# Kernel tuning notes

Measured on AMD Instinct MI355X. Metric: run time of the kernel, lower is better.

## Reference

```python
import jax, jax.numpy as jnp
import numpy as np


def _segsum(v, idx, n):
    return jax.ops.segment_sum(v, idx, num_segments=n)


def _rdl(z, n_dst, Wna, We, Wi, es, ed, is_, id_):
    """Relationship_Decoupled_layer: node softmax attn + per-edge attn.
    e-channel (mode etype): softmax over 2 logits; i-channel: sigmoid(1 logit)."""
    zd = z[:n_dst]
    node_alpha = jax.nn.softmax(zd @ Wna, axis=1)                      # [nd,2]
    e_e = jax.nn.softmax(jnp.concatenate([z[es], zd[ed]], axis=-1) @ We, axis=1)  # [Ee,2]
    e_i = jax.nn.sigmoid(jnp.concatenate([z[is_], zd[id_]], axis=-1) @ Wi)        # [Ei,1]
    return node_alpha, e_e, e_i


def _one_agg(z, n_dst, W, b, na, e_e, es, ed):
    """One_Neighbor_Aggregation: mean over nbrs of e[:,0]*Linear(z_src), relu, + alpha0*z_dst.
    Linear is applied on src nodes once (linearity) instead of per-edge."""
    zd = na[:, 0:1] * z[:n_dst]
    wz = z @ W + b                                                     # [n_src,D]
    s = _segsum(e_e[:, 0:1] * wz[es], ed, n_dst)                       # [nd,D]
    deg = _segsum(jnp.ones((es.shape[0], 1), z.dtype), ed, n_dst)
    f = jax.nn.relu(s / jnp.maximum(deg, 1.0))
    return f + zd


def _nia(z, n_dst, na, e_e, es, ed, e_i, is_, id_):
    """Neighbor_Interaction_Aggregation: e_h (mode etype, attn col 1) and i_h
    (other etype, sigmoid attn), cross term via polarization identity, + alpha1*z_dst."""
    zd = na[:, 1:2] * z[:n_dst]
    e_h = _segsum(e_e[:, 1:2] * z[es], ed, n_dst)
    i_h = _segsum(e_i * z[is_], id_, n_dst)
    inter = jax.nn.relu(0.5 * (jnp.square(e_h + i_h) - jnp.square(e_h) - jnp.square(i_h)))
    return inter + zd


def setup_inputs() -> dict:
    key = jax.random.key(0)
    ks = jax.random.split(key, 32)
    F, D, O = 256, 128, 64
    n_src0, n_dst0, E0 = 100000, 25000, 500000
    n_src1, n_dst1, E1 = 25000, 5000, 100000

    def ri(k, n, hi):
        return jax.random.randint(k, (n,), 0, hi, dtype=jnp.int32)

    inp = {
        'feat': jax.random.normal(ks[0], (n_src0, F), jnp.float32),
        'src0_cor': ri(ks[1], E0, n_src0), 'dst0_cor': ri(ks[2], E0, n_dst0),
        'src0_sim': ri(ks[3], E0, n_src0), 'dst0_sim': ri(ks[4], E0, n_dst0),
        'src1_cor': ri(ks[5], E1, n_src1), 'dst1_cor': ri(ks[6], E1, n_dst1),
        'src1_sim': ri(ks[7], E1, n_src1), 'dst1_sim': ri(ks[8], E1, n_dst1),
        'n_dst0': n_dst0, 'n_dst1': n_dst1,
    }
    s = 0.05  # keep attention logits / activations in a sane range
    inp['Win'] = jax.random.normal(ks[9], (2, F, D)) * s
    inp['b_in'] = jnp.zeros((2, D), jnp.float32)
    inp['na1'] = jax.random.normal(ks[10], (2, D, 2)) * s
    inp['ea1'] = jax.random.normal(ks[11], (2, 2 * D, 2)) * s
    inp['ia1'] = jax.random.normal(ks[12], (2, 2 * D, 1)) * s
    inp['W1'] = jax.random.normal(ks[13], (2, D, D)) * s
    inp['b1'] = jnp.zeros((2, D), jnp.float32)
    inp['na2'] = jax.random.normal(ks[14], (2, D, 2)) * s
    inp['ea2'] = jax.random.normal(ks[15], (2, 2 * D, 2)) * s
    inp['ia2'] = jax.random.normal(ks[16], (2, 2 * D, 1)) * s
    inp['W2'] = jax.random.normal(ks[17], (2, D, D)) * s
    inp['b2'] = jnp.zeros((2, D), jnp.float32)
    inp['Wout'] = jax.random.normal(ks[18], (2, D, O)) * s
    inp['bout'] = jnp.zeros((2, O), jnp.float32)
    return inp


def reference(feat, src0_cor, dst0_cor, src0_sim, dst0_sim,
              src1_cor, dst1_cor, src1_sim, dst1_sim, n_dst0, n_dst1,
              Win, b_in, na1, ea1, ia1, W1, b1, na2, ea2, ia2, W2, b2, Wout, bout):
    # mode index 0 = 'cor', 1 = 'sim'; e-channel = mode etype, i-channel = other etype
    blk0 = {0: (src0_cor, dst0_cor, src0_sim, dst0_sim),
            1: (src0_sim, dst0_sim, src0_cor, dst0_cor)}
    blk1 = {0: (src1_cor, dst1_cor, src1_sim, dst1_sim),
            1: (src1_sim, dst1_sim, src1_cor, dst1_cor)}
    outs = []
    for m in range(2):
        es0, ed0, is0, id0 = blk0[m]
        es1, ed1, is1, id1 = blk1[m]
        z = feat @ Win[m] + b_in[m]                                    # fc_input (eval: dropout = identity)
        # layer 1 on block0
        na, ee, ei = _rdl(z, n_dst0, na1[m], ea1[m], ia1[m], es0, ed0, is0, id0)
        one = _one_agg(z, n_dst0, W1[m], b1[m], na, ee, es0, ed0)
        nia = _nia(z, n_dst0, na, ee, es0, ed0, ei, is0, id0)
        z = 0.5 * (one + nia)                                          # [n_dst0, D]
        # layer 2 on block1
        na, ee, ei = _rdl(z, n_dst1, na2[m], ea2[m], ia2[m], es1, ed1, is1, id1)
        one = _one_agg(z, n_dst1, W2[m], b2[m], na, ee, es1, ed1)
        nia = _nia(z, n_dst1, na, ee, es1, ed1, ei, is1, id1)
        z = 0.5 * (one + nia)                                          # [n_dst1, D]
        outs.append(z @ Wout[m] + bout[m])
    return jnp.stack(outs)                                             # [2, n_dst1, O] (cor, sim)
```

## Files before the change

### kernel.cpp

```cpp
#include <hip/hip_runtime.h>
#include <hip/hip_bf16.h>
#include <math.h>

#define F_DIM 256
#define D_DIM 128
#define O_DIM 64
#define NS0   100000
#define ND0   25000
#define E0_N  500000
#define NS1   25000
#define ND1   5000
#define E1_N  100000

#define NBE0  1954
#define NBE1  391
#define NB_CSR (2 * NBE0 + 2 * NBE1)
#define NB_WPREP 576

typedef __attribute__((ext_vector_type(8))) short s8v;
typedef __attribute__((ext_vector_type(4))) float f4v;

struct CPtr4 { const int *p0, *p1, *p2, *p3; };
struct MPtr4 { int *p0, *p1, *p2, *p3; };

__device__ __forceinline__ float2 unpack2(uint u) {
    union { uint i; float f; } a, b;
    a.i = (u & 0xffffu) << 16; b.i = u & 0xffff0000u;
    return make_float2(a.f, b.f);
}
__device__ __forceinline__ ushort f2bf(float f) {
    __hip_bfloat16 h = __float2bfloat16(f);
    return *(ushort*)&h;
}
__device__ __forceinline__ float u2f(uint u) {
    union { uint i; float f; } v; v.i = u; return v.f;
}
__device__ __forceinline__ uint f2u(float f) {
    union { uint i; float f; } v; v.f = f; return v.i;
}

__global__ __launch_bounds__(256) void gemm_l0(
    const float* __restrict__ A,
    const ushort* __restrict__ Btb,
    const float* __restrict__ biasb,
    ushort* __restrict__ Coutb, size_t coutstr, int M)
{
    constexpr int PA = 40;
    __shared__ ushort As[64 * PA];
    __shared__ ushort Bs[2][128 * PA];

    const int tid = threadIdx.x;
    const int row0 = blockIdx.x * 64;
    const int wave = tid >> 6, lane = tid & 63;
    const int l15 = lane & 15, l4 = lane >> 4;
    const int wm0 = (wave >> 1) * 32;
    const int wn0 = (wave & 1) * 64;

    f4v acc[2][2][4];
    #pragma unroll
    for (int m2 = 0; m2 < 2; ++m2)
        #pragma unroll
        for (int i = 0; i < 2; ++i)
            #pragma unroll
            for (int j = 0; j < 4; ++j)
                acc[m2][i][j] = (f4v)(0.0f);

    for (int kc = 0; kc < F_DIM; kc += 32) {
        __syncthreads();
        {
            int r = tid >> 2, g = (tid & 3) * 8;
            int gr = row0 + r;
            float4 v0 = make_float4(0.f, 0.f, 0.f, 0.f);
            float4 v1 = make_float4(0.f, 0.f, 0.f, 0.f);
            if (gr < M) {
                v0 = *(const float4*)(A + (size_t)gr * F_DIM + kc + g);
                v1 = *(const float4*)(A + (size_t)gr * F_DIM + kc + g + 4);
            }
            ushort4 o0, o1;
            o0.x = f2bf(v0.x); o0.y = f2bf(v0.y); o0.z = f2bf(v0.z); o0.w = f2bf(v0.w);
            o1.x = f2bf(v1.x); o1.y = f2bf(v1.y); o1.z = f2bf(v1.z); o1.w = f2bf(v1.w);
            *(ushort4*)(&As[r * PA + g]) = o0;
            *(ushort4*)(&As[r * PA + g + 4]) = o1;
        }
        #pragma unroll
        for (int m2 = 0; m2 < 2; ++m2)
            #pragma unroll
            for (int it = 0; it < 2; ++it) {
                int f = tid + it * 256;
                int r = f >> 2, g = (f & 3) * 8;
                *(float4*)(&Bs[m2][r * PA + g]) =
                    *(const float4*)(Btb + m2 * (D_DIM * F_DIM) + (size_t)r * F_DIM + kc + g);
            }
        __syncthreads();

        s8v af[2];
        #pragma unroll
        for (int i = 0; i < 2; ++i)
            af[i] = *(const s8v*)(&As[(wm0 + i * 16 + l15) * PA + l4 * 8]);
        #pragma unroll
        for (int m2 = 0; m2 < 2; ++m2) {
            s8v bfr[4];
            #pragma unroll
            for (int j = 0; j < 4; ++j)
                bfr[j] = *(const s8v*)(&Bs[m2][(wn0 + j * 16 + l15) * PA + l4 * 8]);
            #pragma unroll
            for (int i = 0; i < 2; ++i)
                #pragma unroll
                for (int j = 0; j < 4; ++j)
                    acc[m2][i][j] = __builtin_amdgcn_mfma_f32_16x16x32_bf16(
                        af[i], bfr[j], acc[m2][i][j], 0, 0, 0);
        }
    }

    #pragma unroll
    for (int m2 = 0; m2 < 2; ++m2)
        #pragma unroll
        for (int i = 0; i < 2; ++i)
            #pragma unroll
            for (int ii = 0; ii < 4; ++ii) {
                int row = row0 + wm0 + i * 16 + l4 * 4 + ii;
                if (row < M) {
                    #pragma unroll
                    for (int j = 0; j < 4; ++j) {
                        int col = wn0 + j * 16 + l15;
                        Coutb[m2 * coutstr + (size_t)row * D_DIM + col] =
                            f2bf(acc[m2][i][j][ii] + biasb[m2 * D_DIM + col]);
                    }
                }
            }
}

template<int NW, int KD, int EPI>
__global__ __launch_bounds__(256) void mfma_gemm(
    const ushort* __restrict__ Ab, size_t astr,
    const ushort* __restrict__ Btb, size_t btstr,
    const float* __restrict__ biasb, size_t bstr,
    const float* __restrict__ cvecb, size_t cvstr,
    const float* __restrict__ partialb, size_t pstr,
    void* __restrict__ Coutb, size_t coutstr, int M)
{
    const int m = blockIdx.y;
    const ushort* A = Ab + m * astr;
    const ushort* Bt = Btb + m * btstr;
    const float* bias = biasb + m * bstr;
    const float* cvec = (EPI == 2) ? cvecb + m * cvstr : nullptr;
    const float* partial = (EPI == 2) ? partialb + m * pstr : nullptr;
    char* Cout = (char*)Coutb + m * coutstr * (EPI == 1 ? 4 : 2);

    constexpr int PA = 40;
    constexpr int WAVES_M = (NW == 128) ? 2 : 4;
    constexpr int WM = 128 / WAVES_M;
    constexpr int TM = WM / 16;
    constexpr int TN = 4;
    __shared__ ushort As[128 * PA];
    __shared__ ushort Bs[NW * PA];

    const int tid  = threadIdx.x;
    const int row0 = blockIdx.x * 128;
    const int wave = tid >> 6, lane = tid & 63;
    const int l15 = lane & 15, l4 = lane >> 4;
    int wm0, wn0;
    if (NW == 128) { wm0 = (wave >> 1) * 64; wn0 = (wave & 1) * 64; }
    else           { wm0 = wave * WM;        wn0 = 0; }

    f4v acc[TM][TN];
    #pragma unroll
    for (int i = 0; i < TM; ++i)
        #pragma unroll
        for (int j = 0; j < TN; ++j)
            acc[i][j] = (f4v)(0.0f);

    for (int kc = 0; kc < KD; kc += 32) {
        __syncthreads();
        #pragma unroll
        for (int it = 0; it < 2; ++it) {
            int f = tid + it * 256;
            int r = f >> 2, g = (f & 3) * 8;
            int gr = row0 + r;
            float4 v = make_float4(0.f, 0.f, 0.f, 0.f);
            if (gr < M) v = *(const float4*)(A + (size_t)gr * KD + kc + g);
            *(float4*)(&As[r * PA + g]) = v;
        }
        #pragma unroll
        for (int it = 0; it < NW * 32 / (256 * 8); ++it) {
            int f = tid + it * 256;
            int r = f >> 2, g = (f & 3) * 8;
            *(float4*)(&Bs[r * PA + g]) = *(const float4*)(Bt + (size_t)r * KD + kc + g);
        }
        __syncthreads();

        s8v af[TM], bfr[TN];
        #pragma unroll
        for (int i = 0; i < TM; ++i)
            af[i] = *(const s8v*)(&As[(wm0 + i * 16 + l15) * PA + l4 * 8]);
        #pragma unroll
        for (int j = 0; j < TN; ++j)
            bfr[j] = *(const s8v*)(&Bs[(wn0 + j * 16 + l15) * PA + l4 * 8]);
        #pragma unroll
        for (int i = 0; i < TM; ++i)
            #pragma unroll
            for (int j = 0; j < TN; ++j)
                acc[i][j] = __builtin_amdgcn_mfma_f32_16x16x32_bf16(
                    af[i], bfr[j], acc[i][j], 0, 0, 0);
    }

    #pragma unroll
    for (int i = 0; i < TM; ++i) {
        #pragma unroll
        for (int ii = 0; ii < 4; ++ii) {
            int row = row0 + wm0 + i * 16 + l4 * 4 + ii;
            if (row < M) {
                #pragma unroll
                for (int j = 0; j < TN; ++j) {
                    int col = wn0 + j * 16 + l15;
                    float a = acc[i][j][ii];
                    if (EPI == 1) {
                        ((float*)Cout)[(size_t)row * NW + col] = a + bias[col];
                    } else {
                        float val = a + cvec[row] * bias[col];
                        float o = partial[(size_t)row * NW + col] + 0.5f * fmaxf(val, 0.f);
                        ((ushort*)Cout)[(size_t)row * NW + col] = f2bf(o);
                    }
                }
            }
        }
    }
}

__global__ void histo4_prep(CPtr4 ed, MPtr4 cnt,
    const float* __restrict__ Win, const float* __restrict__ W1,
    const float* __restrict__ W2,  const float* __restrict__ Wout,
    ushort* __restrict__ Wtin, ushort* __restrict__ Wt1,
    ushort* __restrict__ Wt2,  ushort* __restrict__ Wtout)
{
    int b = blockIdx.x, t = threadIdx.x;
    if (b >= NB_CSR) {
        int i = (b - NB_CSR) * 256 + t;
        if (i < 65536) {
            int m = i >> 15, r = i & 32767, k = r >> 7, n = r & 127;
            Wtin[m * 32768 + n * 256 + k] = f2bf(Win[m * 32768 + k * 128 + n]);
        } else if (i < 98304) {
            int i2 = i - 65536;
            int m = i2 >> 14, r = i2 & 16383, k = r >> 7, n = r & 127;
            Wt1[m * 16384 + n * 128 + k] = f2bf(W1[m * 16384 + k * 128 + n]);
        } else if (i < 131072) {
            int i2 = i - 98304;
            int m = i2 >> 14, r = i2 & 16383, k = r >> 7, n = r & 127;
            Wt2[m * 16384 + n * 128 + k] = f2bf(W2[m * 16384 + k * 128 + n]);
        } else if (i < 147456) {
            int i2 = i - 131072;
            int m = i2 >> 13, r = i2 & 8191, k = r >> 6, n = r & 63;
            Wtout[m * 8192 + n * 128 + k] = f2bf(Wout[m * 8192 + k * 64 + n]);
        }
        return;
    }
    const int* edp; int* cp; int e, E;
    if (b < NBE0)          { edp = ed.p0; cp = cnt.p0; e = b * 256 + t;              E = E0_N; }
    else if (b < 2 * NBE0) { edp = ed.p1; cp = cnt.p1; e = (b - NBE0) * 256 + t;     E = E0_N; }
    else if (b < 2 * NBE0 + NBE1)
                           { edp = ed.p2; cp = cnt.p2; e = (b - 2 * NBE0) * 256 + t; E = E1_N; }
    else                   { edp = ed.p3; cp = cnt.p3; e = (b - 2 * NBE0 - NBE1) * 256 + t; E = E1_N; }
    if (e < E) atomicAdd(&cp[edp[e]], 1);
}

__global__ __launch_bounds__(1024) void exscan4(MPtr4 cnt, MPtr4 row, MPtr4 head)
{
    __shared__ int part[1024];
    const int b = blockIdx.x, t = threadIdx.x;
    int* cp; int* rp; int* hp; int n;
    if (b == 0)      { cp = cnt.p0; rp = row.p0; hp = head.p0; n = ND0; }
    else if (b == 1) { cp = cnt.p1; rp = row.p1; hp = head.p1; n = ND0; }
    else if (b == 2) { cp = cnt.p2; rp = row.p2; hp = head.p2; n = ND1; }
    else             { cp = cnt.p3; rp = row.p3; hp = head.p3; n = ND1; }

    const int chunk = (n + 1023) >> 10;
    const int start = t * chunk;
    int s = 0;
    for (int i = 0; i < chunk; ++i) {
        int idx = start + i;
        if (idx < n) s += cp[idx];
    }
    part[t] = s;
    __syncthreads();
    for (int off = 1; off < 1024; off <<= 1) {
        int v = (t >= off) ? part[t - off] : 0;
        __syncthreads();
        part[t] += v;
        __syncthreads();
    }
    int run = (t == 0) ? 0 : part[t - 1];
    for (int i = 0; i < chunk; ++i) {
        int idx = start + i;
        if (idx < n) { rp[idx] = run; hp[idx] = run; run += cp[idx]; }
    }
    if (t == 1023) rp[n] = part[1023];
}

__global__ void build4(CPtr4 es, CPtr4 ed, MPtr4 head, MPtr4 src)
{
    int b = blockIdx.x, t = threadIdx.x;
    const int *esp, *edp; int *hp, *sp; int e, E;
    if (b < NBE0)          { esp = es.p0; edp = ed.p0; hp = head.p0; sp = src.p0; e = b * 256 + t;              E = E0_N; }
    else if (b < 2 * NBE0) { esp = es.p1; edp = ed.p1; hp = head.p1; sp = src.p1; e = (b - NBE0) * 256 + t;     E = E0_N; }
    else if (b < 2 * NBE0 + NBE1)
                           { esp = es.p2; edp = ed.p2; hp = head.p2; sp = src.p2; e = (b - 2 * NBE0) * 256 + t; E = E1_N; }
    else                   { esp = es.p3; edp = ed.p3; hp = head.p3; sp = src.p3; e = (b - 2 * NBE0 - NBE1) * 256 + t; E = E1_N; }
    if (e >= E) return;
    int p = atomicAdd(&hp[edp[e]], 1);
    sp[p] = esp[e];
}

#define NP_NPB 128
__global__ __launch_bounds__(256) void node_proj(
    const ushort* __restrict__ zb, size_t zstr,
    const float* __restrict__ Web, const float* __restrict__ Wib,
    float2* __restrict__ pcor, float2* __restrict__ psim,
    float* __restrict__ qcor, float* __restrict__ qsim,
    float* __restrict__ pdb, float* __restrict__ qdb,
    int n_src, int n_dst)
{
    const int m = blockIdx.y;
    const ushort* z = zb + m * zstr;
    const float* We = Web + m * 512;
    const float* Wi = Wib + m * 256;

    __shared__ float w[6][D_DIM];
    for (int k = threadIdx.x; k < D_DIM; k += 256) {
        w[0][k] = We[k * 2 + 0];
        w[1][k] = We[k * 2 + 1];
        w[2][k] = Wi[k];
        w[3][k] = We[(D_DIM + k) * 2 + 0];
        w[4][k] = We[(D_DIM + k) * 2 + 1];
        w[5][k] = Wi[D_DIM + k];
    }
    __syncthreads();

    const int sub = threadIdx.x & 7;
    const int g   = threadIdx.x >> 3;

    float wr[6][16];
    #pragma unroll
    for (int c = 0; c < 6; ++c)
        #pragma unroll
        for (int q = 0; q < 4; ++q) {
            float4 f = *(const float4*)(&w[c][sub * 16 + q * 4]);
            wr[c][q * 4 + 0] = f.x; wr[c][q * 4 + 1] = f.y;
            wr[c][q * 4 + 2] = f.z; wr[c][q * 4 + 3] = f.w;
        }

    #pragma unroll
    for (int it = 0; it < 4; ++it) {
        int node = blockIdx.x * NP_NPB + it * 32 + g;
        if (node >= n_src) continue;
        const ushort* zp = z + (size_t)node * D_DIM + sub * 16;
        uint4 ra = *(const uint4*)zp;
        uint4 rb = *(const uint4*)(zp + 8);
        uint rr[8] = {ra.x, ra.y, ra.z, ra.w, rb.x, rb.y, rb.z, rb.w};
        float p[6] = {0.f, 0.f, 0.f, 0.f, 0.f, 0.f};
        #pragma unroll
        for (int e = 0; e < 8; ++e) {
            float2 f2 = unpack2(rr[e]);
            #pragma unroll
            for (int c = 0; c < 6; ++c)
                p[c] += f2.x * wr[c][2 * e] + f2.y * wr[c][2 * e + 1];
        }
        #pragma unroll
        for (int off = 4; off > 0; off >>= 1)
            #pragma unroll
            for (int c = 0; c < 6; ++c)
                p[c] += __shfl_down(p[c], off);

        if (sub == 0) {
            if (m == 0) {
                pcor[node] = make_float2(p[0], p[1]);
                qsim[node] = p[2];
            } else {
                psim[node] = make_float2(p[0], p[1]);
                qcor[node] = p[2];
            }
            if (node < n_dst) {
                *(float2*)(pdb + (size_t)m * ND0 * 2 + 2 * (size_t)node) = make_float2(p[3], p[4]);
                qdb[(size_t)m * ND0 + node] = p[5];
            }
        }
    }
}

__global__ __launch_bounds__(256) void edge_gather5(
    const ushort* __restrict__ zb, size_t zstr,
    const float2* __restrict__ pcor, const float2* __restrict__ psim,
    const float* __restrict__ qcor, const float* __restrict__ qsim,
    const float* __restrict__ pdb, const float* __restrict__ qdb,
    const int* __restrict__ row_c, const int* __restrict__ src_c,
    const int* __restrict__ row_s, const int* __restrict__ src_s,
    ushort* __restrict__ h0base, float* __restrict__ partialb,
    float* __restrict__ cvecb, int n_dst)
{
    __shared__ uint2 sc[4][64];

    const int m = blockIdx.y;
    const int wv = threadIdx.x >> 6;
    const int d = blockIdx.x * 4 + wv;
    const int lane = threadIdx.x & 63;
    if (d >= n_dst) return;

    const ushort* z = zb + (size_t)m * zstr;
    const ushort* zlane = z + lane * 2;

    const int* erow = m ? row_s : row_c;
    const int* esrc = m ? src_s : src_c;
    const int* irow = m ? row_c : row_s;
    const int* isrc = m ? src_c : src_s;
    const float2* etab = m ? psim : pcor;
    const float*  itab = m ? qcor : qsim;

    const float pd0 = pdb[(size_t)m * ND0 * 2 + 2 * d];
    const float pd1 = pdb[(size_t)m * ND0 * 2 + 2 * d + 1];
    const float qdd = qdb[(size_t)m * ND0 + d];

    float h0x = 0.f, h0y = 0.f, szx = 0.f, szy = 0.f;
    float ihx = 0.f, ihy = 0.f;
    float se0 = 0.f;

    const int b0 = erow[d], b1 = erow[d + 1];
    for (int base = b0; base < b1; base += 64) {
        const int cnt = min(64, b1 - base);
        if (lane < cnt) {
            int s = esrc[base + lane];
            float2 t = etab[s];
            float l0 = t.x + pd0, l1 = t.y + pd1;
            float mx = fmaxf(l0, l1);
            float x0 = __expf(l0 - mx), x1 = __expf(l1 - mx);
            float e0 = x0 / (x0 + x1);
            sc[wv][lane] = make_uint2(f2u(e0), (uint)s);
            se0 += e0;
        }
        asm volatile("s_waitcnt lgkmcnt(0)" ::: "memory");
        const int kf = cnt & ~7;
        int k = 0;
        for (; k < kf; k += 8) {
            uint2 ew[8]; uint rr[8];
            #pragma unroll
            for (int t = 0; t < 8; ++t) ew[t] = sc[wv][k + t];
            #pragma unroll
            for (int t = 0; t < 8; ++t) rr[t] = *(const uint*)(zlane + (size_t)ew[t].y * D_DIM);
            #pragma unroll
            for (int t = 0; t < 8; ++t) {
                float w0 = u2f(ew[t].x);
                float2 v = unpack2(rr[t]);
                szx += v.x; szy += v.y;
                h0x += w0 * v.x; h0y += w0 * v.y;
            }
        }
        if (k < cnt) {
            uint2 ew[8]; uint rr[8];
            #pragma unroll
            for (int t = 0; t < 8; ++t) ew[t] = sc[wv][(k + t) & 63];
            #pragma unroll
            for (int t = 0; t < 8; ++t) {
                uint s = (k + t < cnt) ? ew[t].y : 0u;
                rr[t] = *(const uint*)(zlane + (size_t)s * D_DIM);
            }
            #pragma unroll
            for (int t = 0; t < 8; ++t) {
                float sel = (k + t < cnt) ? 1.0f : 0.0f;
                float w0 = u2f(ew[t].x) * sel;
                float2 v = unpack2(rr[t]);
                szx += v.x * sel; szy += v.y * sel;
                h0x += w0 * v.x; h0y += w0 * v.y;
            }
        }
    }

    #pragma unroll
    for (int off = 32; off > 0; off >>= 1)
        se0 += __shfl_down(se0, off);
    if (lane == 0)
        cvecb[(size_t)m * ND0 + d] = se0 / fmaxf((float)(b1 - b0), 1.0f);

    const int c0 = irow[d], c1 = irow[d + 1];
    for (int base = c0; base < c1; base += 64) {
        const int cnt = min(64, c1 - base);
        if (lane < cnt) {
            int s = isrc[base + lane];
            float ti = itab[s];
            float sg = 1.0f / (1.0f + __expf(-(ti + qdd)));
            sc[wv][lane] = make_uint2(f2u(sg), (uint)s);
        }
        asm volatile("s_waitcnt lgkmcnt(0)" ::: "memory");
        const int kf = cnt & ~7;
        int k = 0;
        for (; k < kf; k += 8) {
            uint2 ew[8]; uint rr[8];
            #pragma unroll
            for (int t = 0; t < 8; ++t) ew[t] = sc[wv][k + t];
            #pragma unroll
            for (int t = 0; t < 8; ++t) rr[t] = *(const uint*)(zlane + (size_t)ew[t].y * D_DIM);
            #pragma unroll
            for (int t = 0; t < 8; ++t) {
                float g = u2f(ew[t].x);
                float2 v = unpack2(rr[t]);
                ihx += g * v.x; ihy += g * v.y;
            }
        }
        if (k < cnt) {
            uint2 ew[8]; uint rr[8];
            #pragma unroll
            for (int t = 0; t < 8; ++t) ew[t] = sc[wv][(k + t) & 63];
            #pragma unroll
            for (int t = 0; t < 8; ++t) {
                uint s = (k + t < cnt) ? ew[t].y : 0u;
                rr[t] = *(const uint*)(zlane + (size_t)s * D_DIM);
            }
            #pragma unroll
            for (int t = 0; t < 8; ++t) {
                float sel = (k + t < cnt) ? 1.0f : 0.0f;
                float g = u2f(ew[t].x) * sel;
                float2 v = unpack2(rr[t]);
                ihx += g * v.x; ihy += g * v.y;
            }
        }
    }

    const int nE = b1 - b0;
    float ehx = szx - h0x, ehy = szy - h0y;
    float inv = 1.0f / fmaxf((float)nE, 1.0f);
    uint hp = (uint)f2bf(h0x * inv) | ((uint)f2bf(h0y * inv) << 16);
    const size_t MSTR = (size_t)ND0 * D_DIM;
    *(uint*)(h0base + (size_t)m * MSTR + (size_t)d * D_DIM + lane * 2) = hp;

    float2 zd = unpack2(*(const uint*)(zlane + (size_t)d * D_DIM));
    float px = 0.5f * (fmaxf(ehx * ihx, 0.f) + zd.x);
    float py = 0.5f * (fmaxf(ehy * ihy, 0.f) + zd.y);
    *(float2*)(partialb + (size_t)m * MSTR + (size_t)d * D_DIM + lane * 2) =
        make_float2(px, py);
}

extern "C" void kernel_launch(void* const* d_in, const int* in_sizes, int n_in,
                              void* d_out, int out_size, void* d_ws, size_t ws_size,
                              hipStream_t stream)
{
    const float* feat = (const float*)d_in[0];
    const int* src0_cor = (const int*)d_in[1];
    const int* dst0_cor = (const int*)d_in[2];
    const int* src0_sim = (const int*)d_in[3];
    const int* dst0_sim = (const int*)d_in[4];
    const int* src1_cor = (const int*)d_in[5];
    const int* dst1_cor = (const int*)d_in[6];
    const int* src1_sim = (const int*)d_in[7];
    const int* dst1_sim = (const int*)d_in[8];
    const float* Win  = (const float*)d_in[11];
    const float* b_in = (const float*)d_in[12];
    const float* ea1  = (const float*)d_in[14];
    const float* ia1  = (const float*)d_in[15];
    const float* W1   = (const float*)d_in[16];
    const float* b1   = (const float*)d_in[17];
    const float* ea2  = (const float*)d_in[19];
    const float* ia2  = (const float*)d_in[20];
    const float* W2   = (const float*)d_in[21];
    const float* b2   = (const float*)d_in[22];
    const float* Wout = (const float*)d_in[23];
    const float* bout = (const float*)d_in[24];
    (void)in_sizes; (void)n_in; (void)out_size; (void)ws_size;

    char* wsb = (char*)d_ws;
    size_t off = 0;
    auto alloc_f  = [&](size_t n) { float*  p = (float*) (wsb + off); off += n * 4; return p; };
    auto alloc_f2 = [&](size_t n) { float2* p = (float2*)(wsb + off); off += n * 8; return p; };
    auto alloc_i  = [&](size_t n) { int*    p = (int*)   (wsb + off); off += n * 4; return p; };
    auto alloc_h  = [&](size_t n) { ushort* p = (ushort*)(wsb + off); off += ((n * 2 + 15) & ~15ull); return p; };

    ushort* z0b   = alloc_h((size_t)2 * NS0 * D_DIM);
    ushort* z1b   = alloc_h((size_t)2 * NS1 * D_DIM);
    ushort* z2b   = alloc_h((size_t)2 * ND1 * D_DIM);
    ushort* h0b   = alloc_h((size_t)2 * ND0 * D_DIM);
    ushort* Wtin  = alloc_h((size_t)2 * D_DIM * F_DIM);
    ushort* Wt1   = alloc_h((size_t)2 * D_DIM * D_DIM);
    ushort* Wt2   = alloc_h((size_t)2 * D_DIM * D_DIM);
    ushort* Wtout = alloc_h((size_t)2 * O_DIM * D_DIM);

    float2* pcor   = alloc_f2((size_t)NS0);
    float2* psim   = alloc_f2((size_t)NS0);
    float* qcor    = alloc_f((size_t)NS0);
    float* qsim    = alloc_f((size_t)NS0);
    float* pd      = alloc_f((size_t)2 * ND0 * 2);
    float* qd      = alloc_f((size_t)2 * ND0);
    float* cvec    = alloc_f((size_t)2 * ND0);
    float* partial = alloc_f((size_t)2 * ND0 * D_DIM);

    int* src_c0 = alloc_i(E0_N); int* row_c0 = alloc_i(ND0 + 1);
    int* src_s0 = alloc_i(E0_N); int* row_s0 = alloc_i(ND0 + 1);
    int* src_c1 = alloc_i(E1_N); int* row_c1 = alloc_i(ND1 + 1);
    int* src_s1 = alloc_i(E1_N); int* row_s1 = alloc_i(ND1 + 1);
    int* cnt_all  = alloc_i(2 * ND0 + 2 * ND1);
    int* head_all = alloc_i(2 * ND0 + 2 * ND1);

    int* cnt_c0 = cnt_all;            int* head_c0 = head_all;
    int* cnt_s0 = cnt_all + ND0;      int* head_s0 = head_all + ND0;
    int* cnt_c1 = cnt_all + 2 * ND0;  int* head_c1 = head_all + 2 * ND0;
    int* cnt_s1 = cnt_c1 + ND1;       int* head_s1 = head_c1 + ND1;

    hipMemsetAsync(cnt_all, 0, (size_t)(2 * ND0 + 2 * ND1) * 4, stream);
    {
        CPtr4 edp  = {dst0_cor, dst0_sim, dst1_cor, dst1_sim};
        CPtr4 esp  = {src0_cor, src0_sim, src1_cor, src1_sim};
        MPtr4 cntp = {cnt_c0, cnt_s0, cnt_c1, cnt_s1};
        MPtr4 rowp = {row_c0, row_s0, row_c1, row_s1};
        MPtr4 hdp  = {head_c0, head_s0, head_c1, head_s1};
        MPtr4 srcp = {src_c0, src_s0, src_c1, src_s1};
        histo4_prep<<<NB_CSR + NB_WPREP, 256, 0, stream>>>(
            edp, cntp, Win, W1, W2, Wout, Wtin, Wt1, Wt2, Wtout);
        exscan4<<<4, 1024, 0, stream>>>(cntp, rowp, hdp);
        build4<<<NB_CSR, 256, 0, stream>>>(esp, edp, hdp, srcp);
    }

    const size_t Z0S = (size_t)NS0 * D_DIM, Z1S = (size_t)NS1 * D_DIM;
    const size_t Z2S = (size_t)ND1 * D_DIM, H0S = (size_t)ND0 * D_DIM;

    gemm_l0<<<(NS0 + 63) / 64, 256, 0, stream>>>(
        feat, Wtin, b_in, z0b, Z0S, NS0);

    node_proj<<<dim3((NS0 + NP_NPB - 1) / NP_NPB, 2), 256, 0, stream>>>(
        z0b, Z0S, ea1, ia1, pcor, psim, qcor, qsim, pd, qd, NS0, ND0);
    edge_gather5<<<dim3((ND0 + 3) / 4, 2), 256, 0, stream>>>(
        z0b, Z0S, pcor, psim, qcor, qsim, pd, qd,
        row_c0, src_c0, row_s0, src_s0, h0b, partial, cvec, ND0);
    mfma_gemm<128, 128, 2><<<dim3((ND0 + 127) / 128, 2), 256, 0, stream>>>(
        h0b, H0S, Wt1, (size_t)D_DIM * D_DIM, b1, D_DIM,
        cvec, ND0, partial, H0S, z1b, Z1S, ND0);

    node_proj<<<dim3((NS1 + NP_NPB - 1) / NP_NPB, 2), 256, 0, stream>>>(
        z1b, Z1S, ea2, ia2, pcor, psim, qcor, qsim, pd, qd, NS1, ND1);
    edge_gather5<<<dim3((ND1 + 3) / 4, 2), 256, 0, stream>>>(
        z1b, Z1S, pcor, psim, qcor, qsim, pd, qd,
        row_c1, src_c1, row_s1, src_s1, h0b, partial, cvec, ND1);
    mfma_gemm<128, 128, 2><<<dim3((ND1 + 127) / 128, 2), 256, 0, stream>>>(
        h0b, H0S, Wt2, (size_t)D_DIM * D_DIM, b2, D_DIM,
        cvec, ND0, partial, H0S, z2b, Z2S, ND1);

    mfma_gemm<64, 128, 1><<<dim3((ND1 + 127) / 128, 2), 256, 0, stream>>>(
        z2b, Z2S, Wtout, (size_t)O_DIM * D_DIM, bout, O_DIM,
        nullptr, 0, nullptr, 0, (float*)d_out, (size_t)ND1 * O_DIM, ND1);
}
```

Before: 538.1 us.

## Fuse CSR build stages into GEMM and node-projection kernels to overlap work

Replaces the memset, histogram/weight-prep, scan, input GEMM and first node-projection launches with three combined kernels. The memset joins weight prep, the destination histogram runs as extra blocks of the input GEMM, and the exclusive scan runs as four extra 256-thread blocks alongside layer-1 node projection. The goal is to cut launch count and let independent CSR work share the GPU with the dense stages. In exchange the scan now uses 256 threads per segment instead of 1024, so each thread walks a longer serial chunk.

```diff
diff --git a/kernel.cpp b/kernel.cpp
--- a/kernel.cpp
+++ b/kernel.cpp
@@ -16,6 +16,9 @@
 #define NBE1  391
 #define NB_CSR (2 * NBE0 + 2 * NBE1)
 #define NB_WPREP 576
+#define NB_MEMSET 235
+#define NB_GEMM0 1563
+#define NB_NP1 782
 
 typedef __attribute__((ext_vector_type(8))) short s8v;
 typedef __attribute__((ext_vector_type(4))) float f4v;
@@ -39,15 +42,60 @@
     union { uint i; float f; } v; v.f = f; return v.i;
 }
 
-__global__ __launch_bounds__(256) void gemm_l0(
+__global__ __launch_bounds__(256) void prep0(
+    int* __restrict__ cnt_all, int ncnt,
+    const float* __restrict__ Win, const float* __restrict__ W1,
+    const float* __restrict__ W2,  const float* __restrict__ Wout,
+    ushort* __restrict__ Wtin, ushort* __restrict__ Wt1,
+    ushort* __restrict__ Wt2,  ushort* __restrict__ Wtout)
+{
+    int b = blockIdx.x, t = threadIdx.x;
+    if (b < NB_MEMSET) {
+        int i = b * 256 + t;
+        if (i < ncnt) cnt_all[i] = 0;
+        return;
+    }
+    int i = (b - NB_MEMSET) * 256 + t;
+    if (i < 65536) {
+        int m = i >> 15, r = i & 32767, k = r >> 7, n = r & 127;
+        Wtin[m * 32768 + n * 256 + k] = f2bf(Win[m * 32768 + k * 128 + n]);
+    } else if (i < 98304) {
+        int i2 = i - 65536;
+        int m = i2 >> 14, r = i2 & 16383, k = r >> 7, n = r & 127;
+        Wt1[m * 16384 + n * 128 + k] = f2bf(W1[m * 16384 + k * 128 + n]);
+    } else if (i < 131072) {
+        int i2 = i - 98304;
+        int m = i2 >> 14, r = i2 & 16383, k = r >> 7, n = r & 127;
+        Wt2[m * 16384 + n * 128 + k] = f2bf(W2[m * 16384 + k * 128 + n]);
+    } else if (i < 147456) {
+        int i2 = i - 131072;
+        int m = i2 >> 13, r = i2 & 8191, k = r >> 6, n = r & 63;
+        Wtout[m * 8192 + n * 128 + k] = f2bf(Wout[m * 8192 + k * 64 + n]);
+    }
+}
+
+__global__ __launch_bounds__(256) void mega1(
     const float* __restrict__ A,
     const ushort* __restrict__ Btb,
     const float* __restrict__ biasb,
-    ushort* __restrict__ Coutb, size_t coutstr, int M)
+    ushort* __restrict__ Coutb, size_t coutstr, int M,
+    CPtr4 ed, MPtr4 cnt)
 {
     constexpr int PA = 40;
     __shared__ ushort As[64 * PA];
     __shared__ ushort Bs[2][128 * PA];
+
+    if (blockIdx.x >= NB_GEMM0) {
+        int b = blockIdx.x - NB_GEMM0, t = threadIdx.x;
+        const int* edp; int* cp; int e, E;
+        if (b < NBE0)          { edp = ed.p0; cp = cnt.p0; e = b * 256 + t;              E = E0_N; }
+        else if (b < 2 * NBE0) { edp = ed.p1; cp = cnt.p1; e = (b - NBE0) * 256 + t;     E = E0_N; }
+        else if (b < 2 * NBE0 + NBE1)
+                               { edp = ed.p2; cp = cnt.p2; e = (b - 2 * NBE0) * 256 + t; E = E1_N; }
+        else                   { edp = ed.p3; cp = cnt.p3; e = (b - 2 * NBE0 - NBE1) * 256 + t; E = E1_N; }
+        if (e < E) atomicAdd(&cp[edp[e]], 1);
+        return;
+    }
 
     const int tid = threadIdx.x;
     const int row0 = blockIdx.x * 64;
@@ -128,6 +176,120 @@
                     }
                 }
             }
+}
+
+#define NP_NPB 128
+__global__ __launch_bounds__(256) void mega2(
+    MPtr4 cnt, MPtr4 row, MPtr4 head,
+    const ushort* __restrict__ zb, size_t zstr,
+    const float* __restrict__ Web, const float* __restrict__ Wib,
+    float2* __restrict__ pcor, float2* __restrict__ psim,
+    float* __restrict__ qcor, float* __restrict__ qsim,
+    float* __restrict__ pdb, float* __restrict__ qdb,
+    int n_src, int n_dst)
+{
+    __shared__ float wsh[6][D_DIM];
+    int* part = (int*)wsh;
+
+    if (blockIdx.x < 4) {
+        const int b = blockIdx.x, t = threadIdx.x;
+        int* cp; int* rp; int* hp; int n;
+        if (b == 0)      { cp = cnt.p0; rp = row.p0; hp = head.p0; n = ND0; }
+        else if (b == 1) { cp = cnt.p1; rp = row.p1; hp = head.p1; n = ND0; }
+        else if (b == 2) { cp = cnt.p2; rp = row.p2; hp = head.p2; n = ND1; }
+        else             { cp = cnt.p3; rp = row.p3; hp = head.p3; n = ND1; }
+
+        const int chunk = (n + 255) >> 8;
+        const int start = t * chunk;
+        int s = 0;
+        for (int i = 0; i < chunk; ++i) {
+            int idx = start + i;
+            if (idx < n) s += cp[idx];
+        }
+        part[t] = s;
+        __syncthreads();
+        for (int off = 1; off < 256; off <<= 1) {
+            int v = (t >= off) ? part[t - off] : 0;
+            __syncthreads();
+            part[t] += v;
+            __syncthreads();
+        }
+        int run = (t == 0) ? 0 : part[t - 1];
+        for (int i = 0; i < chunk; ++i) {
+            int idx = start + i;
+            if (idx < n) { rp[idx] = run; hp[idx] = run; run += cp[idx]; }
+        }
+        if (t == 255) rp[n] = part[255];
+        return;
+    }
+
+    const int bb = blockIdx.x - 4;
+    const int m = (bb < NB_NP1) ? 0 : 1;
+    const int bx = bb - (m ? NB_NP1 : 0);
+
+    const ushort* z = zb + (size_t)m * zstr;
+    const float* We = Web + m * 512;
+    const float* Wi = Wib + m * 256;
+
+    for (int k = threadIdx.x; k < D_DIM; k += 256) {
+        wsh[0][k] = We[k * 2 + 0];
+        wsh[1][k] = We[k * 2 + 1];
+        wsh[2][k] = Wi[k];
+        wsh[3][k] = We[(D_DIM + k) * 2 + 0];
+        wsh[4][k] = We[(D_DIM + k) * 2 + 1];
+        wsh[5][k] = Wi[D_DIM + k];
+    }
+    __syncthreads();
+
+    const int sub = threadIdx.x & 7;
+    const int g   = threadIdx.x >> 3;
+
+    float wr[6][16];
+    #pragma unroll
+    for (int c = 0; c < 6; ++c)
+        #pragma unroll
+        for (int q = 0; q < 4; ++q) {
+            float4 f = *(const float4*)(&wsh[c][sub * 16 + q * 4]);
+            wr[c][q * 4 + 0] = f.x; wr[c][q * 4 + 1] = f.y;
+            wr[c][q * 4 + 2] = f.z; wr[c][q * 4 + 3] = f.w;
+        }
+
+    #pragma unroll
+    for (int it = 0; it < 4; ++it) {
+        int node = bx * NP_NPB + it * 32 + g;
+        if (node >= n_src) continue;
+        const ushort* zp = z + (size_t)node * D_DIM + sub * 16;
+        uint4 ra = *(const uint4*)zp;
+        uint4 rb = *(const uint4*)(zp + 8);
+        uint rr[8] = {ra.x, ra.y, ra.z, ra.w, rb.x, rb.y, rb.z, rb.w};
+        float p[6] = {0.f, 0.f, 0.f, 0.f, 0.f, 0.f};
+        #pragma unroll
+        for (int e = 0; e < 8; ++e) {
+            float2 f2 = unpack2(rr[e]);
+            #pragma unroll
+            for (int c = 0; c < 6; ++c)
+                p[c] += f2.x * wr[c][2 * e] + f2.y * wr[c][2 * e + 1];
+        }
+        #pragma unroll
+        for (int off = 4; off > 0; off >>= 1)
+            #pragma unroll
+            for (int c = 0; c < 6; ++c)
+                p[c] += __shfl_down(p[c], off);
+
+        if (sub == 0) {
+            if (m == 0) {
+                pcor[node] = make_float2(p[0], p[1]);
+                qsim[node] = p[2];
+            } else {
+                psim[node] = make_float2(p[0], p[1]);
+                qcor[node] = p[2];
+            }
+            if (node < n_dst) {
+                *(float2*)(pdb + (size_t)m * ND0 * 2 + 2 * (size_t)node) = make_float2(p[3], p[4]);
+                qdb[(size_t)m * ND0 + node] = p[5];
+            }
+        }
+    }
 }
 
 template<int NW, int KD, int EPI>
@@ -227,75 +389,6 @@
     }
 }
 
-__global__ void histo4_prep(CPtr4 ed, MPtr4 cnt,
-    const float* __restrict__ Win, const float* __restrict__ W1,
-    const float* __restrict__ W2,  const float* __restrict__ Wout,
-    ushort* __restrict__ Wtin, ushort* __restrict__ Wt1,
-    ushort* __restrict__ Wt2,  ushort* __restrict__ Wtout)
-{
-    int b = blockIdx.x, t = threadIdx.x;
-    if (b >= NB_CSR) {
-        int i = (b - NB_CSR) * 256 + t;
-        if (i < 65536) {
-            int m = i >> 15, r = i & 32767, k = r >> 7, n = r & 127;
-            Wtin[m * 32768 + n * 256 + k] = f2bf(Win[m * 32768 + k * 128 + n]);
-        } else if (i < 98304) {
-            int i2 = i - 65536;
-            int m = i2 >> 14, r = i2 & 16383, k = r >> 7, n = r & 127;
-            Wt1[m * 16384 + n * 128 + k] = f2bf(W1[m * 16384 + k * 128 + n]);
-        } else if (i < 131072) {
-            int i2 = i - 98304;
-            int m = i2 >> 14, r = i2 & 16383, k = r >> 7, n = r & 127;
-            Wt2[m * 16384 + n * 128 + k] = f2bf(W2[m * 16384 + k * 128 + n]);
-        } else if (i < 147456) {
-            int i2 = i - 131072;
-            int m = i2 >> 13, r = i2 & 8191, k = r >> 6, n = r & 63;
-            Wtout[m * 8192 + n * 128 + k] = f2bf(Wout[m * 8192 + k * 64 + n]);
-        }
-        return;
-    }
-    const int* edp; int* cp; int e, E;
-    if (b < NBE0)          { edp = ed.p0; cp = cnt.p0; e = b * 256 + t;              E = E0_N; }
-    else if (b < 2 * NBE0) { edp = ed.p1; cp = cnt.p1; e = (b - NBE0) * 256 + t;     E = E0_N; }
-    else if (b < 2 * NBE0 + NBE1)
-                           { edp = ed.p2; cp = cnt.p2; e = (b - 2 * NBE0) * 256 + t; E = E1_N; }
-    else                   { edp = ed.p3; cp = cnt.p3; e = (b - 2 * NBE0 - NBE1) * 256 + t; E = E1_N; }
-    if (e < E) atomicAdd(&cp[edp[e]], 1);
-}
-
-__global__ __launch_bounds__(1024) void exscan4(MPtr4 cnt, MPtr4 row, MPtr4 head)
-{
-    __shared__ int part[1024];
-    const int b = blockIdx.x, t = threadIdx.x;
-    int* cp; int* rp; int* hp; int n;
-    if (b == 0)      { cp = cnt.p0; rp = row.p0; hp = head.p0; n = ND0; }
-    else if (b == 1) { cp = cnt.p1; rp = row.p1; hp = head.p1; n = ND0; }
-    else if (b == 2) { cp = cnt.p2; rp = row.p2; hp = head.p2; n = ND1; }
-    else             { cp = cnt.p3; rp = row.p3; hp = head.p3; n = ND1; }
-
-    const int chunk = (n + 1023) >> 10;
-    const int start = t * chunk;
-    int s = 0;
-    for (int i = 0; i < chunk; ++i) {
-        int idx = start + i;
-        if (idx < n) s += cp[idx];
-    }
-    part[t] = s;
-    __syncthreads();
-    for (int off = 1; off < 1024; off <<= 1) {
-        int v = (t >= off) ? part[t - off] : 0;
-        __syncthreads();
-        part[t] += v;
-        __syncthreads();
-    }
-    int run = (t == 0) ? 0 : part[t - 1];
-    for (int i = 0; i < chunk; ++i) {
-        int idx = start + i;
-        if (idx < n) { rp[idx] = run; hp[idx] = run; run += cp[idx]; }
-    }
-    if (t == 1023) rp[n] = part[1023];
-}
-
 __global__ void build4(CPtr4 es, CPtr4 ed, MPtr4 head, MPtr4 src)
 {
     int b = blockIdx.x, t = threadIdx.x;
@@ -310,7 +403,6 @@
     sp[p] = esp[e];
 }
 
-#define NP_NPB 128
 __global__ __launch_bounds__(256) void node_proj(
     const ushort* __restrict__ zb, size_t zstr,
     const float* __restrict__ Web, const float* __restrict__ Wib,
@@ -600,28 +692,28 @@
     int* cnt_c1 = cnt_all + 2 * ND0;  int* head_c1 = head_all + 2 * ND0;
     int* cnt_s1 = cnt_c1 + ND1;       int* head_s1 = head_c1 + ND1;
 
-    hipMemsetAsync(cnt_all, 0, (size_t)(2 * ND0 + 2 * ND1) * 4, stream);
-    {
-        CPtr4 edp  = {dst0_cor, dst0_sim, dst1_cor, dst1_sim};
-        CPtr4 esp  = {src0_cor, src0_sim, src1_cor, src1_sim};
-        MPtr4 cntp = {cnt_c0, cnt_s0, cnt_c1, cnt_s1};
-        MPtr4 rowp = {row_c0, row_s0, row_c1, row_s1};
-        MPtr4 hdp  = {head_c0, head_s0, head_c1, head_s1};
-        MPtr4 srcp = {src_c0, src_s0, src_c1, src_s1};
-        histo4_prep<<<NB_CSR + NB_WPREP, 256, 0, stream>>>(
-            edp, cntp, Win, W1, W2, Wout, Wtin, Wt1, Wt2, Wtout);
-        exscan4<<<4, 1024, 0, stream>>>(cntp, rowp, hdp);
-        build4<<<NB_CSR, 256, 0, stream>>>(esp, edp, hdp, srcp);
-    }
+    CPtr4 edp  = {dst0_cor, dst0_sim, dst1_cor, dst1_sim};
+    CPtr4 esp  = {src0_cor, src0_sim, src1_cor, src1_sim};
+    MPtr4 cntp = {cnt_c0, cnt_s0, cnt_c1, cnt_s1};
+    MPtr4 rowp = {row_c0, row_s0, row_c1, row_s1};
+    MPtr4 hdp  = {head_c0, head_s0, head_c1, head_s1};
+    MPtr4 srcp = {src_c0, src_s0, src_c1, src_s1};
 
     const size_t Z0S = (size_t)NS0 * D_DIM, Z1S = (size_t)NS1 * D_DIM;
     const size_t Z2S = (size_t)ND1 * D_DIM, H0S = (size_t)ND0 * D_DIM;
 
-    gemm_l0<<<(NS0 + 63) / 64, 256, 0, stream>>>(
-        feat, Wtin, b_in, z0b, Z0S, NS0);
-
-    node_proj<<<dim3((NS0 + NP_NPB - 1) / NP_NPB, 2), 256, 0, stream>>>(
+    prep0<<<NB_MEMSET + NB_WPREP, 256, 0, stream>>>(
+        cnt_all, 2 * ND0 + 2 * ND1, Win, W1, W2, Wout, Wtin, Wt1, Wt2, Wtout);
+
+    mega1<<<NB_GEMM0 + NB_CSR, 256, 0, stream>>>(
+        feat, Wtin, b_in, z0b, Z0S, NS0, edp, cntp);
+
+    mega2<<<4 + 2 * NB_NP1, 256, 0, stream>>>(
+        cntp, rowp, hdp,
         z0b, Z0S, ea1, ia1, pcor, psim, qcor, qsim, pd, qd, NS0, ND0);
+
+    build4<<<NB_CSR, 256, 0, stream>>>(esp, edp, hdp, srcp);
+
     edge_gather5<<<dim3((ND0 + 3) / 4, 2), 256, 0, stream>>>(
         z0b, Z0S, pcor, psim, qcor, qsim, pd, qd,
         row_c0, src_c0, row_s0, src_s0, h0b, partial, cvec, ND0);
```

After: 545.2 us. No clear change (+1.3%).
